# Performance work log

Hardware: AMD Instinct MI355X
Metric: run time of the kernel (lower is better)

Reference implementation:

```python
import jax, jax.numpy as jnp
import numpy as np

N_NODES = 200000
N_EDGES = 5000000
NUM_FEATURES = 16
DIM = 10
NUM_GRAPHS = 1000


def _glorot(key, shape):
    fan_in, fan_out = shape[0], shape[1]
    lim = np.sqrt(6.0 / (fan_in + fan_out)).astype(np.float32)
    return jax.random.uniform(key, shape, jnp.float32, -lim, lim)


def setup_inputs() -> dict:
    key = jax.random.key(0)
    ks = jax.random.split(key, 16)
    x = jax.random.normal(ks[0], (N_NODES, NUM_FEATURES), jnp.float32)
    edge_index = jax.random.randint(ks[1], (2, N_EDGES), 0, N_NODES, jnp.int32)
    batch = jnp.sort(jax.random.randint(ks[2], (N_NODES,), 0, NUM_GRAPHS, jnp.int32))
    # conv1 MLP: Linear(num_features, dim) -> ReLU -> Linear(dim, dim)
    w1_1 = _glorot(ks[3], (NUM_FEATURES, DIM))
    b1_1 = jnp.zeros((DIM,), jnp.float32)
    w2_1 = _glorot(ks[4], (DIM, DIM))
    b2_1 = jnp.zeros((DIM,), jnp.float32)
    # conv2..conv5 MLPs stacked: [4, dim, dim]
    ws1 = jnp.stack([_glorot(ks[5 + i], (DIM, DIM)) for i in range(4)])
    bs1 = jnp.zeros((4, DIM), jnp.float32)
    ws2 = jnp.stack([_glorot(ks[9 + i], (DIM, DIM)) for i in range(4)])
    bs2 = jnp.zeros((4, DIM), jnp.float32)
    # l1..l5: Linear(dim, 1, bias=False), stacked [5, dim]
    lw = jax.random.normal(ks[13], (5, DIM), jnp.float32) * (1.0 / np.sqrt(DIM))
    return {"x": x, "edge_index": edge_index, "batch": batch,
            "w1_1": w1_1, "b1_1": b1_1, "w2_1": w2_1, "b2_1": b2_1,
            "ws1": ws1, "bs1": bs1, "ws2": ws2, "bs2": bs2, "lw": lw}


def _gin_conv(h, src, dst, w1, b1, w2, b2):
    # GINConv with eps=0: nn((1+eps)*x + sum_{j in N(i)} x_j)
    agg = jnp.zeros_like(h).at[dst].add(h[src])  # scatter-add over edges
    z = h + agg
    z = jax.nn.relu(z @ w1 + b1) @ w2 + b2
    return z


def reference(x, edge_index, batch, w1_1, b1_1, w2_1, b2_1, ws1, bs1, ws2, bs2, lw):
    src, dst = edge_index[0], edge_index[1]
    x1 = jax.nn.relu(_gin_conv(x, src, dst, w1_1, b1_1, w2_1, b2_1))
    x2 = jax.nn.relu(_gin_conv(x1, src, dst, ws1[0], bs1[0], ws2[0], bs2[0]))
    x3 = jax.nn.relu(_gin_conv(x2, src, dst, ws1[1], bs1[1], ws2[1], bs2[1]))
    x4 = jax.nn.relu(_gin_conv(x3, src, dst, ws1[2], bs1[2], ws2[2], bs2[2]))
    x5 = jax.nn.relu(_gin_conv(x4, src, dst, ws1[3], bs1[3], ws2[3], bs2[3]))
    counts = jax.ops.segment_sum(jnp.ones((x.shape[0],), x.dtype), batch,
                                 num_segments=NUM_GRAPHS)
    denom = jnp.maximum(counts, 1.0)[:, None]  # [G, 1]

    def mean_pool(h):
        return jax.ops.segment_sum(h, batch, num_segments=NUM_GRAPHS) / denom

    # sum_i l_i(mean_pool(x_i)) -> [G, 1]
    ms = jnp.stack([mean_pool(x1), mean_pool(x2), mean_pool(x3),
                    mean_pool(x4), mean_pool(x5)])  # [5, G, dim]
    out = jnp.einsum('lgd,ld->g', ms, lw)[:, None]
    return jax.nn.sigmoid(out)
```

## Files before the change

### kernel.cpp

```cpp
#include <hip/hip_runtime.h>
#include <math.h>

#define N_NODES 200000
#define N_EDGES 5000000
#define NFEAT 16
#define DIM 10
#define NGRAPH 1000
#define BSH 8
#define BNODES 256
#define NB ((N_NODES + BNODES - 1) / BNODES)
#define NBLK 512
#define STB 512
#define RSTRIDE 5

__device__ __forceinline__ unsigned pkbf(float a, float b) {
    unsigned ua = __float_as_uint(a), ub = __float_as_uint(b);
    ua = (ua + 0x7fffu + ((ua >> 16) & 1u)) >> 16;
    ub = (ub + 0x7fffu + ((ub >> 16) & 1u)) >> 16;
    return ua | (ub << 16);
}
__device__ __forceinline__ float uplo(unsigned u) { return __uint_as_float(u << 16); }
__device__ __forceinline__ float uphi(unsigned u) { return __uint_as_float(u & 0xffff0000u); }

__global__ void __launch_bounds__(STB)
khist(const int* __restrict__ dst, unsigned* __restrict__ histg,
      unsigned* __restrict__ tot) {
    __shared__ int h[NB];
    for (int t = threadIdx.x; t < NB; t += STB) h[t] = 0;
    __syncthreads();
    int per = (N_EDGES + NBLK - 1) / NBLK;
    int e0 = blockIdx.x * per;
    int e1 = e0 + per; if (e1 > N_EDGES) e1 = N_EDGES;
    int e = e0 + threadIdx.x;
    for (; e + 7 * STB < e1; e += 8 * STB) {
        int d[8];
#pragma unroll
        for (int k = 0; k < 8; ++k) d[k] = __builtin_nontemporal_load(&dst[e + k * STB]);
#pragma unroll
        for (int k = 0; k < 8; ++k) atomicAdd(&h[d[k] >> BSH], 1);
    }
    for (; e < e1; e += STB)
        atomicAdd(&h[__builtin_nontemporal_load(&dst[e]) >> BSH], 1);
    __syncthreads();
    for (int t = threadIdx.x; t < NB; t += STB) {
        int c = h[t];
        histg[(size_t)blockIdx.x * NB + t] = c;
        if (c) atomicAdd(&tot[t], (unsigned)c);
    }
}

__global__ void __launch_bounds__(1024)
kscan_tot(const unsigned* __restrict__ tot, int* __restrict__ bstart) {
    __shared__ int s[NB];
    int t = threadIdx.x;
    if (t < NB) s[t] = tot[t];
    __syncthreads();
    if (t == 0) {
        int acc = 0;
        for (int i = 0; i < NB; ++i) { int c = s[i]; s[i] = acc; acc += c; }
    }
    __syncthreads();
    if (t < NB) bstart[t] = s[t];
    if (t == 0) bstart[NB] = N_EDGES;
}

__global__ void __launch_bounds__(STB)
kscan_wb(unsigned* __restrict__ histg, const int* __restrict__ bstart) {
    int t = blockIdx.x;
    int tid = threadIdx.x;
    int lane = tid & 63, wv = tid >> 6;
    unsigned v = histg[(size_t)tid * NB + t];
    unsigned orig = v;
#pragma unroll
    for (int m = 1; m < 64; m <<= 1) {
        unsigned u = __shfl(v, lane - m, 64);
        if (lane >= m) v += u;
    }
    __shared__ unsigned wtot[8];
    __shared__ unsigned wbase[8];
    if (lane == 63) wtot[wv] = v;
    __syncthreads();
    if (tid == 0) {
        unsigned acc = 0;
        for (int w = 0; w < 8; ++w) { wbase[w] = acc; acc += wtot[w]; }
    }
    __syncthreads();
    unsigned excl = v - orig + wbase[wv];
    histg[(size_t)tid * NB + t] = (unsigned)bstart[t] + excl;
}

__global__ void __launch_bounds__(STB)
kscatter(const int* __restrict__ src, const int* __restrict__ dst,
         const unsigned* __restrict__ histg, unsigned* __restrict__ packed) {
    __shared__ int wp[NB];
    for (int t = threadIdx.x; t < NB; t += STB)
        wp[t] = histg[(size_t)blockIdx.x * NB + t];
    __syncthreads();
    int per = (N_EDGES + NBLK - 1) / NBLK;
    int e0 = blockIdx.x * per;
    int e1 = e0 + per; if (e1 > N_EDGES) e1 = N_EDGES;
    int e = e0 + threadIdx.x;
    for (; e + 7 * STB < e1; e += 8 * STB) {
        int d[8], s[8];
#pragma unroll
        for (int k = 0; k < 8; ++k) {
            d[k] = __builtin_nontemporal_load(&dst[e + k * STB]);
            s[k] = __builtin_nontemporal_load(&src[e + k * STB]);
        }
#pragma unroll
        for (int k = 0; k < 8; ++k) {
            int r = atomicAdd(&wp[d[k] >> BSH], 1);
            packed[r] = ((unsigned)s[k] << BSH) | (unsigned)(d[k] & (BNODES - 1));
        }
    }
    for (; e < e1; e += STB) {
        int dv = __builtin_nontemporal_load(&dst[e]);
        int sv = __builtin_nontemporal_load(&src[e]);
        int r = atomicAdd(&wp[dv >> BSH], 1);
        packed[r] = ((unsigned)sv << BSH) | (unsigned)(dv & (BNODES - 1));
    }
}

__global__ void __launch_bounds__(BNODES)
node_sort(const unsigned* __restrict__ pin, const int* __restrict__ bstart,
          unsigned* __restrict__ ecol, int* __restrict__ rowstart) {
    __shared__ int cnt[BNODES];
    __shared__ int cur[BNODES];
    int b = blockIdx.x;
    int e0 = bstart[b], e1 = bstart[b + 1];
    int tid = threadIdx.x;
    cnt[tid] = 0;
    __syncthreads();
    int e = e0 + tid;
    for (; e + 7 * BNODES < e1; e += 8 * BNODES) {
        unsigned p[8];
#pragma unroll
        for (int k = 0; k < 8; ++k) p[k] = __builtin_nontemporal_load(&pin[e + k * BNODES]);
#pragma unroll
        for (int k = 0; k < 8; ++k) atomicAdd(&cnt[p[k] & (BNODES - 1)], 1);
    }
    for (; e < e1; e += BNODES)
        atomicAdd(&cnt[__builtin_nontemporal_load(&pin[e]) & (BNODES - 1)], 1);
    __syncthreads();
    if (tid == 0) {
        int acc = 0;
        for (int t = 0; t < BNODES; ++t) { int c = cnt[t]; cur[t] = acc; acc += c; }
    }
    __syncthreads();
    int n0 = b << BSH;
    if (n0 + tid < N_NODES) rowstart[n0 + tid] = e0 + cur[tid];
    if (b == 0 && tid == 0) rowstart[N_NODES] = N_EDGES;
    e = e0 + tid;
    for (; e + 3 * BNODES < e1; e += 4 * BNODES) {
        unsigned p[4];
#pragma unroll
        for (int k = 0; k < 4; ++k) p[k] = __builtin_nontemporal_load(&pin[e + k * BNODES]);
#pragma unroll
        for (int k = 0; k < 4; ++k) {
            int slot = atomicAdd(&cur[p[k] & (BNODES - 1)], 1);
            ecol[e0 + slot] = p[k] >> BSH;
        }
    }
    for (; e < e1; e += BNODES) {
        unsigned p = __builtin_nontemporal_load(&pin[e]);
        int slot = atomicAdd(&cur[p & (BNODES - 1)], 1);
        ecol[e0 + slot] = p >> BSH;
    }
}

__global__ void xform_kernel(const float* __restrict__ x,
                             const float* __restrict__ w1,
                             unsigned* __restrict__ tout) {
    int i = blockIdx.x * blockDim.x + threadIdx.x;
    if (i >= N_NODES) return;
    float xi[NFEAT];
    const float4* xr = reinterpret_cast<const float4*>(x + (size_t)i * NFEAT);
#pragma unroll
    for (int q = 0; q < 4; q++) {
        float4 v = xr[q];
        xi[q*4+0] = v.x; xi[q*4+1] = v.y; xi[q*4+2] = v.z; xi[q*4+3] = v.w;
    }
    float o[DIM];
#pragma unroll
    for (int j = 0; j < DIM; j++) {
        float s = 0.f;
#pragma unroll
        for (int f = 0; f < NFEAT; f++) s += xi[f] * w1[f * DIM + j];
        o[j] = s;
    }
#pragma unroll
    for (int k = 0; k < 5; k++)
        __builtin_nontemporal_store(pkbf(o[2*k], o[2*k+1]),
                                    &tout[(size_t)RSTRIDE * i + k]);
}

template <bool FIRST>
__global__ void __launch_bounds__(256, 8)
gin_gatherE(const unsigned* __restrict__ tin,
            const int* __restrict__ rowstart,
            const unsigned* __restrict__ ecol,
            const float* __restrict__ w1, const float* __restrict__ b1,
            const float* __restrict__ w2, const float* __restrict__ b2,
            const int* __restrict__ batch,
            unsigned* __restrict__ tout,
            float* __restrict__ pooled) {
    __shared__ float hp[16][DIM];
    __shared__ int gid[16];
    int tid = threadIdx.x;
    int grp = tid >> 4;
    int j = tid & 15;
    int lane = tid & 63;
    int base = lane & 48;
    int i = blockIdx.x * 16 + grp;

    int r0 = rowstart[i];
    int r1 = rowstart[i + 1];

    float a[DIM];
#pragma unroll
    for (int d = 0; d < DIM; ++d) a[d] = 0.f;

    int idx = r0 + j;
    for (; idx + 16 < r1; idx += 32) {
        unsigned sA = __builtin_nontemporal_load(&ecol[idx]);
        unsigned sB = __builtin_nontemporal_load(&ecol[idx + 16]);
        const unsigned* rA = tin + (size_t)sA * RSTRIDE;
        const unsigned* rB = tin + (size_t)sB * RSTRIDE;
        unsigned wA[5], wB[5];
#pragma unroll
        for (int k = 0; k < 5; ++k) wA[k] = rA[k];
#pragma unroll
        for (int k = 0; k < 5; ++k) wB[k] = rB[k];
#pragma unroll
        for (int k = 0; k < 5; ++k) {
            a[2*k]   += uplo(wA[k]) + uplo(wB[k]);
            a[2*k+1] += uphi(wA[k]) + uphi(wB[k]);
        }
    }
    if (idx < r1) {
        unsigned sA = __builtin_nontemporal_load(&ecol[idx]);
        const unsigned* rA = tin + (size_t)sA * RSTRIDE;
        unsigned wA[5];
#pragma unroll
        for (int k = 0; k < 5; ++k) wA[k] = rA[k];
#pragma unroll
        for (int k = 0; k < 5; ++k) {
            a[2*k]   += uplo(wA[k]);
            a[2*k+1] += uphi(wA[k]);
        }
    }

#pragma unroll
    for (int m = 1; m <= 8; m <<= 1) {
#pragma unroll
        for (int d = 0; d < DIM; ++d) a[d] += __shfl_xor(a[d], m, 64);
    }

    const unsigned* ri = tin + (size_t)i * RSTRIDE;
    float z[DIM];
#pragma unroll
    for (int k = 0; k < 5; ++k) {
        unsigned w = ri[k];
        z[2*k]   = uplo(w) + a[2*k];
        z[2*k+1] = uphi(w) + a[2*k+1];
    }

    float t1v = 0.f;
    if (FIRST) {
        if (j < DIM) {
            float s1 = z[j] + b1[j];
            t1v = s1 > 0.f ? s1 : 0.f;
        }
    } else {
        if (j < DIM) {
            float s1 = b1[j];
#pragma unroll
            for (int f = 0; f < DIM; ++f) s1 += z[f] * w1[f * DIM + j];
            t1v = s1 > 0.f ? s1 : 0.f;
        }
    }
    float s2 = (j < DIM) ? b2[j] : 0.f;
#pragma unroll
    for (int f = 0; f < DIM; ++f) {
        float tf = __shfl(t1v, base + f, 64);
        if (j < DIM) s2 += tf * w2[f * DIM + j];
    }
    float hv = s2 > 0.f ? s2 : 0.f;

    float hnext = __shfl(hv, base + ((j + 1) & 15), 64);
    if (j < DIM && !(j & 1))
        __builtin_nontemporal_store(pkbf(hv, hnext), &tout[(size_t)i * RSTRIDE + (j >> 1)]);

    if (j < DIM) hp[grp][j] = hv;
    if (j == 0) gid[grp] = batch[i];
    __syncthreads();

    if (tid < DIM) {
        int cg = gid[0];
        float s = hp[0][tid];
        for (int n = 1; n < 16; ++n) {
            int g = gid[n];
            float v = hp[n][tid];
            if (g == cg) s += v;
            else { atomicAdd(&pooled[cg * DIM + tid], s); cg = g; s = v; }
        }
        atomicAdd(&pooled[cg * DIM + tid], s);
    }
}

__global__ void final_kernel(const float* __restrict__ pooled,
                             const int* __restrict__ batch,
                             const float* __restrict__ lw,
                             float* __restrict__ out) {
    int g = blockIdx.x * blockDim.x + threadIdx.x;
    if (g >= NGRAPH) return;
    int lo = 0, hi = N_NODES;
    while (lo < hi) { int m = (lo + hi) >> 1; if (batch[m] < g) lo = m + 1; else hi = m; }
    int a = lo;
    hi = N_NODES;
    while (lo < hi) { int m = (lo + hi) >> 1; if (batch[m] < g + 1) lo = m + 1; else hi = m; }
    float c = (float)(lo - a);
    float inv = 1.0f / (c > 1.f ? c : 1.f);
    float s = 0.f;
#pragma unroll
    for (int l = 0; l < 5; l++) {
        float d = 0.f;
#pragma unroll
        for (int j = 0; j < DIM; j++)
            d += pooled[(size_t)l * NGRAPH * DIM + (size_t)g * DIM + j] * lw[l * DIM + j];
        s += d * inv;
    }
    out[g] = 1.0f / (1.0f + expf(-s));
}

extern "C" void kernel_launch(void* const* d_in, const int* in_sizes, int n_in,
                              void* d_out, int out_size, void* d_ws, size_t ws_size,
                              hipStream_t stream) {
    const float* x    = (const float*)d_in[0];
    const int*   ei   = (const int*)d_in[1];
    const int*   batch= (const int*)d_in[2];
    const float* w1_1 = (const float*)d_in[3];
    const float* b1_1 = (const float*)d_in[4];
    const float* w2_1 = (const float*)d_in[5];
    const float* b2_1 = (const float*)d_in[6];
    const float* ws1  = (const float*)d_in[7];
    const float* bs1  = (const float*)d_in[8];
    const float* ws2  = (const float*)d_in[9];
    const float* bs2  = (const float*)d_in[10];
    const float* lw   = (const float*)d_in[11];
    float* out = (float*)d_out;

    const int* src = ei;
    const int* dst = ei + N_EDGES;

    int* bstart      = (int*)d_ws;
    unsigned* tot    = (unsigned*)d_ws + 784;
    int* rowstart    = (int*)d_ws + 1568;
    unsigned* histg  = (unsigned*)d_ws + 201584;
    unsigned* packed = histg + (size_t)NBLK * NB;
    unsigned* tA1    = packed;
    unsigned* ecol   = packed + N_EDGES;
    unsigned* tA0    = ecol + N_EDGES;
    float* pooled    = (float*)(tA0 + (size_t)N_NODES * RSTRIDE);
    size_t needed = (size_t)((char*)(pooled + 5 * NGRAPH * DIM) - (char*)d_ws);
    if (needed > ws_size) return;

    const int TB = 256;
    int nblocks = (N_NODES + TB - 1) / TB;
    int gblocks = (NGRAPH + TB - 1) / TB;

    hipMemsetAsync(tot, 0, NB * sizeof(unsigned), stream);
    hipMemsetAsync(pooled, 0, (size_t)5 * NGRAPH * DIM * sizeof(float), stream);

    khist<<<NBLK, STB, 0, stream>>>(dst, histg, tot);
    kscan_tot<<<1, 1024, 0, stream>>>(tot, bstart);
    kscan_wb<<<NB, STB, 0, stream>>>(histg, bstart);
    kscatter<<<NBLK, STB, 0, stream>>>(src, dst, histg, packed);
    node_sort<<<NB, BNODES, 0, stream>>>(packed, bstart, ecol, rowstart);

    xform_kernel<<<nblocks, TB, 0, stream>>>(x, w1_1, tA0);
    gin_gatherE<true><<<N_NODES / 16, TB, 0, stream>>>(tA0, rowstart, ecol,
        nullptr, b1_1, w2_1, b2_1, batch, tA1, pooled);

    unsigned *tin = tA1, *tout2 = tA0;
    for (int l = 0; l < 4; l++) {
        gin_gatherE<false><<<N_NODES / 16, TB, 0, stream>>>(tin, rowstart, ecol,
            ws1 + (size_t)l * DIM * DIM, bs1 + (size_t)l * DIM,
            ws2 + (size_t)l * DIM * DIM, bs2 + (size_t)l * DIM,
            batch, tout2, pooled + (size_t)(l + 1) * NGRAPH * DIM);
        unsigned* t = tin; tin = tout2; tout2 = t;
    }

    final_kernel<<<gblocks, TB, 0, stream>>>(pooled, batch, lw, out);
}
```

Measured before the change: 465.0 us.

## Stage radix-sort scatter in LDS for coalesced global writes

The coarse scatter kernel now does a per-block local sort in shared memory. It computes local bucket offsets from the histogram, writes edges into an LDS staging buffer grouped by bucket, then copies them out contiguously to global memory using precomputed per-bucket adjustments. The node-level sort likewise stages each bucket's edges in LDS, falling back to direct writes when a bucket exceeds capacity. The aim is to replace random scattered global stores with mostly coalesced ones, at the cost of large shared-memory use (about 49KB per scatter block), which lowers occupancy, plus an extra buffer for the write bases.

```diff
diff --git a/kernel.cpp b/kernel.cpp
--- a/kernel.cpp
+++ b/kernel.cpp
@@ -11,6 +11,8 @@
 #define NB ((N_NODES + BNODES - 1) / BNODES)
 #define NBLK 512
 #define STB 512
+#define CH ((N_EDGES + NBLK - 1) / NBLK)
+#define NSCAP 8192
 #define RSTRIDE 5
 
 __device__ __forceinline__ unsigned pkbf(float a, float b) {
@@ -28,9 +30,8 @@
     __shared__ int h[NB];
     for (int t = threadIdx.x; t < NB; t += STB) h[t] = 0;
     __syncthreads();
-    int per = (N_EDGES + NBLK - 1) / NBLK;
-    int e0 = blockIdx.x * per;
-    int e1 = e0 + per; if (e1 > N_EDGES) e1 = N_EDGES;
+    int e0 = blockIdx.x * CH;
+    int e1 = e0 + CH; if (e1 > N_EDGES) e1 = N_EDGES;
     int e = e0 + threadIdx.x;
     for (; e + 7 * STB < e1; e += 8 * STB) {
         int d[8];
@@ -65,7 +66,8 @@
 }
 
 __global__ void __launch_bounds__(STB)
-kscan_wb(unsigned* __restrict__ histg, const int* __restrict__ bstart) {
+kscan_wb(const unsigned* __restrict__ histg, unsigned* __restrict__ wbaseg,
+         const int* __restrict__ bstart) {
     int t = blockIdx.x;
     int tid = threadIdx.x;
     int lane = tid & 63, wv = tid >> 6;
@@ -86,38 +88,73 @@
     }
     __syncthreads();
     unsigned excl = v - orig + wbase[wv];
-    histg[(size_t)tid * NB + t] = (unsigned)bstart[t] + excl;
+    wbaseg[(size_t)tid * NB + t] = (unsigned)bstart[t] + excl;
 }
 
 __global__ void __launch_bounds__(STB)
 kscatter(const int* __restrict__ src, const int* __restrict__ dst,
-         const unsigned* __restrict__ histg, unsigned* __restrict__ packed) {
-    __shared__ int wp[NB];
-    for (int t = threadIdx.x; t < NB; t += STB)
-        wp[t] = histg[(size_t)blockIdx.x * NB + t];
-    __syncthreads();
-    int per = (N_EDGES + NBLK - 1) / NBLK;
-    int e0 = blockIdx.x * per;
-    int e1 = e0 + per; if (e1 > N_EDGES) e1 = N_EDGES;
-    int e = e0 + threadIdx.x;
-    for (; e + 7 * STB < e1; e += 8 * STB) {
-        int d[8], s[8];
-#pragma unroll
-        for (int k = 0; k < 8; ++k) {
-            d[k] = __builtin_nontemporal_load(&dst[e + k * STB]);
-            s[k] = __builtin_nontemporal_load(&src[e + k * STB]);
-        }
-#pragma unroll
-        for (int k = 0; k < 8; ++k) {
-            int r = atomicAdd(&wp[d[k] >> BSH], 1);
-            packed[r] = ((unsigned)s[k] << BSH) | (unsigned)(d[k] & (BNODES - 1));
-        }
-    }
-    for (; e < e1; e += STB) {
-        int dv = __builtin_nontemporal_load(&dst[e]);
-        int sv = __builtin_nontemporal_load(&src[e]);
-        int r = atomicAdd(&wp[dv >> BSH], 1);
-        packed[r] = ((unsigned)sv << BSH) | (unsigned)(dv & (BNODES - 1));
+         const unsigned* __restrict__ histg, const unsigned* __restrict__ wbaseg,
+         unsigned* __restrict__ packed) {
+    __shared__ unsigned stage[CH];
+    __shared__ unsigned short bkt16[CH];
+    __shared__ int cur[NB];
+    __shared__ int wadj[NB];
+    __shared__ int wtot[8], wbase2[8];
+    int tid = threadIdx.x;
+    int blk = blockIdx.x;
+    int e0 = blk * CH;
+    int e1 = e0 + CH; if (e1 > N_EDGES) e1 = N_EDGES;
+    int cnt = e1 - e0;
+
+    int i0 = 2 * tid, i1 = 2 * tid + 1;
+    int a0 = (i0 < NB) ? (int)histg[(size_t)blk * NB + i0] : 0;
+    int a1 = (i1 < NB) ? (int)histg[(size_t)blk * NB + i1] : 0;
+    int s = a0 + a1;
+    int lane = tid & 63, wv = tid >> 6;
+    int v = s;
+#pragma unroll
+    for (int m = 1; m < 64; m <<= 1) {
+        int u = __shfl(v, lane - m, 64);
+        if (lane >= m) v += u;
+    }
+    if (lane == 63) wtot[wv] = v;
+    __syncthreads();
+    if (tid == 0) { int acc = 0; for (int w = 0; w < 8; ++w) { wbase2[w] = acc; acc += wtot[w]; } }
+    __syncthreads();
+    int excl = v - s + wbase2[wv];
+    if (i0 < NB) { cur[i0] = excl;      wadj[i0] = (int)wbaseg[(size_t)blk * NB + i0] - excl; }
+    if (i1 < NB) { cur[i1] = excl + a0; wadj[i1] = (int)wbaseg[(size_t)blk * NB + i1] - (excl + a0); }
+    __syncthreads();
+
+    int p = tid;
+    for (; p + 3 * STB < cnt; p += 4 * STB) {
+        int d[4], sv[4];
+#pragma unroll
+        for (int k = 0; k < 4; ++k) {
+            d[k]  = __builtin_nontemporal_load(&dst[e0 + p + k * STB]);
+            sv[k] = __builtin_nontemporal_load(&src[e0 + p + k * STB]);
+        }
+#pragma unroll
+        for (int k = 0; k < 4; ++k) {
+            int t = d[k] >> BSH;
+            int pos = atomicAdd(&cur[t], 1);
+            stage[pos] = ((unsigned)sv[k] << BSH) | (unsigned)(d[k] & (BNODES - 1));
+            bkt16[pos] = (unsigned short)t;
+        }
+    }
+    for (; p < cnt; p += STB) {
+        int d = __builtin_nontemporal_load(&dst[e0 + p]);
+        int sv = __builtin_nontemporal_load(&src[e0 + p]);
+        int t = d >> BSH;
+        int pos = atomicAdd(&cur[t], 1);
+        stage[pos] = ((unsigned)sv << BSH) | (unsigned)(d & (BNODES - 1));
+        bkt16[pos] = (unsigned short)t;
+    }
+    __syncthreads();
+
+    for (int q = tid; q < cnt; q += STB) {
+        int t = bkt16[q];
+        packed[wadj[t] + q] = stage[q];
     }
 }
 
@@ -126,8 +163,10 @@
           unsigned* __restrict__ ecol, int* __restrict__ rowstart) {
     __shared__ int cnt[BNODES];
     __shared__ int cur[BNODES];
+    __shared__ unsigned stage[NSCAP];
     int b = blockIdx.x;
     int e0 = bstart[b], e1 = bstart[b + 1];
+    int n = e1 - e0;
     int tid = threadIdx.x;
     cnt[tid] = 0;
     __syncthreads();
@@ -150,21 +189,32 @@
     int n0 = b << BSH;
     if (n0 + tid < N_NODES) rowstart[n0 + tid] = e0 + cur[tid];
     if (b == 0 && tid == 0) rowstart[N_NODES] = N_EDGES;
-    e = e0 + tid;
-    for (; e + 3 * BNODES < e1; e += 4 * BNODES) {
-        unsigned p[4];
-#pragma unroll
-        for (int k = 0; k < 4; ++k) p[k] = __builtin_nontemporal_load(&pin[e + k * BNODES]);
-#pragma unroll
-        for (int k = 0; k < 4; ++k) {
-            int slot = atomicAdd(&cur[p[k] & (BNODES - 1)], 1);
-            ecol[e0 + slot] = p[k] >> BSH;
-        }
-    }
-    for (; e < e1; e += BNODES) {
-        unsigned p = __builtin_nontemporal_load(&pin[e]);
-        int slot = atomicAdd(&cur[p & (BNODES - 1)], 1);
-        ecol[e0 + slot] = p >> BSH;
+    if (n <= NSCAP) {
+        e = e0 + tid;
+        for (; e + 3 * BNODES < e1; e += 4 * BNODES) {
+            unsigned p[4];
+#pragma unroll
+            for (int k = 0; k < 4; ++k) p[k] = __builtin_nontemporal_load(&pin[e + k * BNODES]);
+#pragma unroll
+            for (int k = 0; k < 4; ++k) {
+                int slot = atomicAdd(&cur[p[k] & (BNODES - 1)], 1);
+                stage[slot] = p[k] >> BSH;
+            }
+        }
+        for (; e < e1; e += BNODES) {
+            unsigned p = __builtin_nontemporal_load(&pin[e]);
+            int slot = atomicAdd(&cur[p & (BNODES - 1)], 1);
+            stage[slot] = p >> BSH;
+        }
+        __syncthreads();
+        for (int q = tid; q < n; q += BNODES) ecol[e0 + q] = stage[q];
+    } else {
+        e = e0 + tid;
+        for (; e < e1; e += BNODES) {
+            unsigned p = __builtin_nontemporal_load(&pin[e]);
+            int slot = atomicAdd(&cur[p & (BNODES - 1)], 1);
+            ecol[e0 + slot] = p >> BSH;
+        }
     }
 }
 
@@ -357,7 +407,8 @@
     unsigned* tot    = (unsigned*)d_ws + 784;
     int* rowstart    = (int*)d_ws + 1568;
     unsigned* histg  = (unsigned*)d_ws + 201584;
-    unsigned* packed = histg + (size_t)NBLK * NB;
+    unsigned* wbaseg = histg + (size_t)NBLK * NB;
+    unsigned* packed = wbaseg + (size_t)NBLK * NB;
     unsigned* tA1    = packed;
     unsigned* ecol   = packed + N_EDGES;
     unsigned* tA0    = ecol + N_EDGES;
@@ -374,8 +425,8 @@
 
     khist<<<NBLK, STB, 0, stream>>>(dst, histg, tot);
     kscan_tot<<<1, 1024, 0, stream>>>(tot, bstart);
-    kscan_wb<<<NB, STB, 0, stream>>>(histg, bstart);
-    kscatter<<<NBLK, STB, 0, stream>>>(src, dst, histg, packed);
+    kscan_wb<<<NB, STB, 0, stream>>>(histg, wbaseg, bstart);
+    kscatter<<<NBLK, STB, 0, stream>>>(src, dst, histg, wbaseg, packed);
     node_sort<<<NB, BNODES, 0, stream>>>(packed, bstart, ecol, rowstart);
 
     xform_kernel<<<nblocks, TB, 0, stream>>>(x, w1_1, tA0);
```

After: 398.3 us (median of 2 runs). 14.4% less time.
